# Kernel optimization log

Measured on AMD Instinct MI355X. Metric: run time of the kernel, lower is better.

The kernel has to match this reference:

```python
import jax, jax.numpy as jnp
import numpy as np

EPS = 1e-05

def _q(a):
    # 'bfloat16' set_precision: round to bf16, compute in fp32
    return a.astype(jnp.bfloat16).astype(jnp.float32)

def setup_inputs() -> dict:
    key = jax.random.key(0)
    k1, k2 = jax.random.split(key)
    B, C, H, W = 64, 128, 56, 56
    x = jax.random.normal(k1, (B, C, H, W), dtype=jnp.float32)
    gamma = jax.random.uniform(k2, (C,), dtype=jnp.float32)
    beta = jnp.zeros((C,), dtype=jnp.float32)
    return {"x": x, "gamma": gamma, "beta": beta, "num_chunks": 8}

def reference(x, gamma, beta, num_chunks):
    B, C, H, W = x.shape
    x = _q(x)
    g = _q(gamma)
    # (C, num_chunks, B*H*W/num_chunks): channel-major flatten then chunk
    y = jnp.transpose(x, (1, 0, 2, 3)).reshape(C, num_chunks, -1)
    chunk_size = y.shape[-1]
    sum_max = _q(y.max(-1).sum(-1))            # [C]
    sum_min = _q(y.min(-1).sum(-1))            # [C]
    avg_max = _q(sum_max / num_chunks)
    avg_min = _q(sum_min / num_chunks)
    total = _q(y.reshape(C, -1).sum(-1))       # [C]
    n = B * H * W
    avg = _q(total / n)
    scale_fix = 1.0 / (2.0 * np.log(chunk_size)) ** 0.5
    scale = _q(1.0 / ((avg_max - avg_min) * scale_fix + EPS))
    avg = avg.reshape(1, C, 1, 1)
    scale = scale.reshape(1, C, 1, 1)
    out = _q((x - avg) * scale)
    out = _q(out * g.reshape(1, C, 1, 1) + beta.reshape(1, C, 1, 1))
    return out
```

## Files before the change

kernel.cpp:

```cpp
#include <hip/hip_runtime.h>
#include <hip/hip_bf16.h>
#include <math.h>

constexpr int HW = 56 * 56;

__device__ __forceinline__ float qbf(float f) {
    unsigned u = __float_as_uint(f);
    u += 0x7fffu + ((u >> 16) & 1u);
    u &= 0xffff0000u;
    return __uint_as_float(u);
}

__global__ __launch_bounds__(256) void stats_kernel(
    const float* __restrict__ x, const int* __restrict__ nch_p,
    int C, int n,
    float* __restrict__ ws_max, float* __restrict__ ws_min, float* __restrict__ ws_sum)
{
    const int nch = *nch_p;
    const int cs  = n / nch;
    const int P   = C * nch;

    __shared__ float smax[4], smin[4], ssum[4];

    for (int p = blockIdx.x; p < P; p += gridDim.x) {
        const int c = p / nch;
        const int j = p - c * nch;

        float vmax = -INFINITY, vmin = INFINITY, vsum = 0.f;

        if ((cs & 3) == 0) {
            const int cs4 = cs >> 2;
            for (int t = threadIdx.x; t < cs4; t += blockDim.x) {
                const int f = j * cs + 4 * t;
                const int b = f / HW;
                const int r = f - b * HW;
                const float4 v = *reinterpret_cast<const float4*>(
                    x + ((size_t)b * C + c) * HW + r);
                const float a0 = qbf(v.x), a1 = qbf(v.y), a2 = qbf(v.z), a3 = qbf(v.w);
                vmax = fmaxf(vmax, fmaxf(fmaxf(a0, a1), fmaxf(a2, a3)));
                vmin = fminf(vmin, fminf(fminf(a0, a1), fminf(a2, a3)));
                vsum += (a0 + a1) + (a2 + a3);
            }
        } else {
            for (int t = threadIdx.x; t < cs; t += blockDim.x) {
                const int f = j * cs + t;
                const int b = f / HW;
                const int r = f - b * HW;
                const float a = qbf(x[((size_t)b * C + c) * HW + r]);
                vmax = fmaxf(vmax, a);
                vmin = fminf(vmin, a);
                vsum += a;
            }
        }

        #pragma unroll
        for (int off = 32; off > 0; off >>= 1) {
            vmax = fmaxf(vmax, __shfl_xor(vmax, off));
            vmin = fminf(vmin, __shfl_xor(vmin, off));
            vsum += __shfl_xor(vsum, off);
        }
        const int wave = threadIdx.x >> 6;
        if ((threadIdx.x & 63) == 0) { smax[wave] = vmax; smin[wave] = vmin; ssum[wave] = vsum; }
        __syncthreads();
        if (threadIdx.x == 0) {
            float m = smax[0], mi = smin[0], s = ssum[0];
            const int nw = blockDim.x >> 6;
            for (int w = 1; w < nw; ++w) {
                m = fmaxf(m, smax[w]); mi = fminf(mi, smin[w]); s += ssum[w];
            }
            ws_max[p] = m; ws_min[p] = mi; ws_sum[p] = s;
        }
        __syncthreads();
    }
}

__global__ __launch_bounds__(256) void finalize_kernel(
    const float* __restrict__ ws_max, const float* __restrict__ ws_min,
    const float* __restrict__ ws_sum, const int* __restrict__ nch_p,
    int C, int n, float* __restrict__ avg_out, float* __restrict__ scale_out)
{
    const int c = blockIdx.x * blockDim.x + threadIdx.x;
    if (c >= C) return;
    const int nch = *nch_p;

    float smax = 0.f, smin = 0.f, stot = 0.f;
    for (int j = 0; j < nch; ++j) {
        smax += ws_max[c * nch + j];
        smin += ws_min[c * nch + j];
        stot += ws_sum[c * nch + j];
    }
    smax = qbf(smax);
    smin = qbf(smin);
    const float avg_max = qbf(smax / (float)nch);
    const float avg_min = qbf(smin / (float)nch);
    const float total   = qbf(stot);
    const float avg     = qbf(total / (float)n);

    const int cs = n / nch;
    const double sf_d = 1.0 / sqrt(2.0 * log((double)cs));
    const float scale_fix = (float)sf_d;
    const float scale = qbf(1.0f / ((avg_max - avg_min) * scale_fix + 1e-5f));

    avg_out[c]   = avg;
    scale_out[c] = scale;
}

__global__ __launch_bounds__(256) void norm_kernel(
    const float* __restrict__ x, const float* __restrict__ gamma,
    const float* __restrict__ beta, const float* __restrict__ avg,
    const float* __restrict__ scale, int C, long total, float* __restrict__ out)
{
    const long total4 = total >> 2;
    const long stride = (long)gridDim.x * blockDim.x;
    for (long i4 = (long)blockIdx.x * blockDim.x + threadIdx.x; i4 < total4; i4 += stride) {
        const long i = i4 << 2;
        const int  c = (int)((i / HW) % C);
        const float a = avg[c], s = scale[c], g = qbf(gamma[c]), bt = beta[c];
        const float4 v = *reinterpret_cast<const float4*>(x + i);
        float4 o;
        o.x = qbf(qbf((qbf(v.x) - a) * s) * g + bt);
        o.y = qbf(qbf((qbf(v.y) - a) * s) * g + bt);
        o.z = qbf(qbf((qbf(v.z) - a) * s) * g + bt);
        o.w = qbf(qbf((qbf(v.w) - a) * s) * g + bt);
        *reinterpret_cast<float4*>(out + i) = o;
    }
    const long rem_start = total4 << 2;
    if (blockIdx.x == 0) {
        for (long i = rem_start + threadIdx.x; i < total; i += blockDim.x) {
            const int c = (int)((i / HW) % C);
            const float a = avg[c], s = scale[c], g = qbf(gamma[c]), bt = beta[c];
            out[i] = qbf(qbf((qbf(x[i]) - a) * s) * g + bt);
        }
    }
}

extern "C" void kernel_launch(void* const* d_in, const int* in_sizes, int n_in,
                              void* d_out, int out_size, void* d_ws, size_t ws_size,
                              hipStream_t stream) {
    const float* x     = (const float*)d_in[0];
    const float* gamma = (const float*)d_in[1];
    const float* beta  = (const float*)d_in[2];
    const int*   nch_p = (const int*)d_in[3];
    float* out = (float*)d_out;

    const int  C     = in_sizes[1];
    const long total = (long)in_sizes[0];
    const int  n     = (int)(total / C);

    constexpr int Pmax = 4096, Cmax = 1024;
    float* ws_f   = (float*)d_ws;
    float* ws_max = ws_f;
    float* ws_min = ws_f + Pmax;
    float* ws_sum = ws_f + 2 * Pmax;
    float* avg    = ws_f + 3 * Pmax;
    float* scale  = ws_f + 3 * Pmax + Cmax;

    stats_kernel<<<1024, 256, 0, stream>>>(x, nch_p, C, n, ws_max, ws_min, ws_sum);
    finalize_kernel<<<(C + 255) / 256, 256, 0, stream>>>(ws_max, ws_min, ws_sum,
                                                         nch_p, C, n, avg, scale);
    norm_kernel<<<2048, 256, 0, stream>>>(x, gamma, beta, avg, scale, C, total, out);
}
```

Baseline: 201.7 us.

## Fuse stats, finalize and normalize into one cooperative kernel with grid syncs

Replaces the three separate launches with a single cooperative kernel that computes per-chunk stats, grid-syncs, has block 0 finalize per-channel avg/scale, grid-syncs again, then normalizes. It also switches to plane-wise indexing in both stats and normalize passes, which avoids per-element divisions by HW, and the normalize pass hoists per-channel parameters out of the inner loop. This removes launch gaps and may let x stay partly in cache between passes. In exchange it adds two grid-wide barriers, a serial finalize step on one block, and a fixed 1024-block grid that must be co-resident.

```diff
diff --git a/kernel.cpp b/kernel.cpp
--- a/kernel.cpp
+++ b/kernel.cpp
@@ -1,8 +1,12 @@
 #include <hip/hip_runtime.h>
 #include <hip/hip_bf16.h>
+#include <hip/hip_cooperative_groups.h>
 #include <math.h>
 
-constexpr int HW = 56 * 56;
+namespace cg = cooperative_groups;
+
+constexpr int HW  = 56 * 56;
+constexpr int HW4 = HW / 4;
 
 __device__ __forceinline__ float qbf(float f) {
     unsigned u = __float_as_uint(f);
@@ -11,16 +15,30 @@
     return __uint_as_float(u);
 }
 
-__global__ __launch_bounds__(256) void stats_kernel(
-    const float* __restrict__ x, const int* __restrict__ nch_p,
-    int C, int n,
-    float* __restrict__ ws_max, float* __restrict__ ws_min, float* __restrict__ ws_sum)
+constexpr int WS_MAX = 0;
+constexpr int WS_MIN = 4096;
+constexpr int WS_SUM = 8192;
+constexpr int WS_AVG = 12288;
+constexpr int WS_SCL = 13312;
+
+__global__ __launch_bounds__(256, 4) void fused_kernel(
+    const float* __restrict__ x, const float* __restrict__ gamma,
+    const float* __restrict__ beta, const int* __restrict__ nch_p,
+    int C, int n, unsigned total, float* __restrict__ ws, float* __restrict__ out)
 {
     const int nch = *nch_p;
     const int cs  = n / nch;
     const int P   = C * nch;
 
+    float* ws_max = ws + WS_MAX;
+    float* ws_min = ws + WS_MIN;
+    float* ws_sum = ws + WS_SUM;
+    float* avgv   = ws + WS_AVG;
+    float* sclv   = ws + WS_SCL;
+
     __shared__ float smax[4], smin[4], ssum[4];
+
+    const bool plane_mode = (cs % HW == 0) && ((total % (unsigned)HW) == 0u);
 
     for (int p = blockIdx.x; p < P; p += gridDim.x) {
         const int c = p / nch;
@@ -28,14 +46,15 @@
 
         float vmax = -INFINITY, vmin = INFINITY, vsum = 0.f;
 
-        if ((cs & 3) == 0) {
-            const int cs4 = cs >> 2;
-            for (int t = threadIdx.x; t < cs4; t += blockDim.x) {
-                const int f = j * cs + 4 * t;
-                const int b = f / HW;
-                const int r = f - b * HW;
+        if (plane_mode) {
+            const int ppc  = cs / HW;
+            const int b0   = j * ppc;
+            const int tot4 = ppc * HW4;
+            for (int t = threadIdx.x; t < tot4; t += blockDim.x) {
+                const int b = t / HW4;
+                const int r = t - b * HW4;
                 const float4 v = *reinterpret_cast<const float4*>(
-                    x + ((size_t)b * C + c) * HW + r);
+                    x + ((size_t)(b0 + b) * C + c) * HW + 4 * r);
                 const float a0 = qbf(v.x), a1 = qbf(v.y), a2 = qbf(v.z), a3 = qbf(v.w);
                 vmax = fmaxf(vmax, fmaxf(fmaxf(a0, a1), fmaxf(a2, a3)));
                 vmin = fminf(vmin, fminf(fminf(a0, a1), fminf(a2, a3)));
@@ -64,71 +83,62 @@
         __syncthreads();
         if (threadIdx.x == 0) {
             float m = smax[0], mi = smin[0], s = ssum[0];
-            const int nw = blockDim.x >> 6;
-            for (int w = 1; w < nw; ++w) {
+            for (int w = 1; w < 4; ++w) {
                 m = fmaxf(m, smax[w]); mi = fminf(mi, smin[w]); s += ssum[w];
             }
             ws_max[p] = m; ws_min[p] = mi; ws_sum[p] = s;
         }
         __syncthreads();
     }
-}
 
-__global__ __launch_bounds__(256) void finalize_kernel(
-    const float* __restrict__ ws_max, const float* __restrict__ ws_min,
-    const float* __restrict__ ws_sum, const int* __restrict__ nch_p,
-    int C, int n, float* __restrict__ avg_out, float* __restrict__ scale_out)
-{
-    const int c = blockIdx.x * blockDim.x + threadIdx.x;
-    if (c >= C) return;
-    const int nch = *nch_p;
+    cg::this_grid().sync();
 
-    float smax = 0.f, smin = 0.f, stot = 0.f;
-    for (int j = 0; j < nch; ++j) {
-        smax += ws_max[c * nch + j];
-        smin += ws_min[c * nch + j];
-        stot += ws_sum[c * nch + j];
+    if (blockIdx.x == 0) {
+        for (int c = threadIdx.x; c < C; c += blockDim.x) {
+            float smx = 0.f, smn = 0.f, stot = 0.f;
+            for (int j = 0; j < nch; ++j) {
+                smx  += ws_max[c * nch + j];
+                smn  += ws_min[c * nch + j];
+                stot += ws_sum[c * nch + j];
+            }
+            smx = qbf(smx);
+            smn = qbf(smn);
+            const float avg_max = qbf(smx / (float)nch);
+            const float avg_min = qbf(smn / (float)nch);
+            const float tq      = qbf(stot);
+            const float avg     = qbf(tq / (float)n);
+            const double sf_d   = 1.0 / sqrt(2.0 * log((double)cs));
+            const float scale_fix = (float)sf_d;
+            const float scale = qbf(1.0f / ((avg_max - avg_min) * scale_fix + 1e-5f));
+            avgv[c] = avg;
+            sclv[c] = scale;
+        }
     }
-    smax = qbf(smax);
-    smin = qbf(smin);
-    const float avg_max = qbf(smax / (float)nch);
-    const float avg_min = qbf(smin / (float)nch);
-    const float total   = qbf(stot);
-    const float avg     = qbf(total / (float)n);
 
-    const int cs = n / nch;
-    const double sf_d = 1.0 / sqrt(2.0 * log((double)cs));
-    const float scale_fix = (float)sf_d;
-    const float scale = qbf(1.0f / ((avg_max - avg_min) * scale_fix + 1e-5f));
+    cg::this_grid().sync();
 
-    avg_out[c]   = avg;
-    scale_out[c] = scale;
-}
-
-__global__ __launch_bounds__(256) void norm_kernel(
-    const float* __restrict__ x, const float* __restrict__ gamma,
-    const float* __restrict__ beta, const float* __restrict__ avg,
-    const float* __restrict__ scale, int C, long total, float* __restrict__ out)
-{
-    const long total4 = total >> 2;
-    const long stride = (long)gridDim.x * blockDim.x;
-    for (long i4 = (long)blockIdx.x * blockDim.x + threadIdx.x; i4 < total4; i4 += stride) {
-        const long i = i4 << 2;
-        const int  c = (int)((i / HW) % C);
-        const float a = avg[c], s = scale[c], g = qbf(gamma[c]), bt = beta[c];
-        const float4 v = *reinterpret_cast<const float4*>(x + i);
-        float4 o;
-        o.x = qbf(qbf((qbf(v.x) - a) * s) * g + bt);
-        o.y = qbf(qbf((qbf(v.y) - a) * s) * g + bt);
-        o.z = qbf(qbf((qbf(v.z) - a) * s) * g + bt);
-        o.w = qbf(qbf((qbf(v.w) - a) * s) * g + bt);
-        *reinterpret_cast<float4*>(out + i) = o;
-    }
-    const long rem_start = total4 << 2;
-    if (blockIdx.x == 0) {
-        for (long i = rem_start + threadIdx.x; i < total; i += blockDim.x) {
-            const int c = (int)((i / HW) % C);
-            const float a = avg[c], s = scale[c], g = qbf(gamma[c]), bt = beta[c];
+    if (plane_mode) {
+        const int planes = (int)(total / (unsigned)HW);
+        for (int pl = blockIdx.x; pl < planes; pl += gridDim.x) {
+            const int c = pl % C;
+            const float a = avgv[c], s = sclv[c], g = qbf(gamma[c]), bt = beta[c];
+            const float* xp = x   + (size_t)pl * HW;
+            float*       op = out + (size_t)pl * HW;
+            for (int t = threadIdx.x; t < HW4; t += blockDim.x) {
+                const float4 v = *reinterpret_cast<const float4*>(xp + 4 * t);
+                float4 o;
+                o.x = qbf(qbf((qbf(v.x) - a) * s) * g + bt);
+                o.y = qbf(qbf((qbf(v.y) - a) * s) * g + bt);
+                o.z = qbf(qbf((qbf(v.z) - a) * s) * g + bt);
+                o.w = qbf(qbf((qbf(v.w) - a) * s) * g + bt);
+                *reinterpret_cast<float4*>(op + 4 * t) = o;
+            }
+        }
+    } else {
+        const unsigned stride = gridDim.x * blockDim.x;
+        for (unsigned i = blockIdx.x * blockDim.x + threadIdx.x; i < total; i += stride) {
+            const int c = (int)((i / (unsigned)HW) % (unsigned)C);
+            const float a = avgv[c], s = sclv[c], g = qbf(gamma[c]), bt = beta[c];
             out[i] = qbf(qbf((qbf(x[i]) - a) * s) * g + bt);
         }
     }
@@ -141,22 +151,15 @@
     const float* gamma = (const float*)d_in[1];
     const float* beta  = (const float*)d_in[2];
     const int*   nch_p = (const int*)d_in[3];
-    float* out = (float*)d_out;
+    float* outp = (float*)d_out;
+    float* ws   = (float*)d_ws;
 
-    const int  C     = in_sizes[1];
-    const long total = (long)in_sizes[0];
-    const int  n     = (int)(total / C);
+    const int      C     = in_sizes[1];
+    const unsigned total = (unsigned)in_sizes[0];
+    const int      n     = (int)(total / (unsigned)C);
 
-    constexpr int Pmax = 4096, Cmax = 1024;
-    float* ws_f   = (float*)d_ws;
-    float* ws_max = ws_f;
-    float* ws_min = ws_f + Pmax;
-    float* ws_sum = ws_f + 2 * Pmax;
-    float* avg    = ws_f + 3 * Pmax;
-    float* scale  = ws_f + 3 * Pmax + Cmax;
-
-    stats_kernel<<<1024, 256, 0, stream>>>(x, nch_p, C, n, ws_max, ws_min, ws_sum);
-    finalize_kernel<<<(C + 255) / 256, 256, 0, stream>>>(ws_max, ws_min, ws_sum,
-                                                         nch_p, C, n, avg, scale);
-    norm_kernel<<<2048, 256, 0, stream>>>(x, gamma, beta, avg, scale, C, total, out);
+    void* args[] = { (void*)&x, (void*)&gamma, (void*)&beta, (void*)&nch_p,
+                     (void*)&C, (void*)&n, (void*)&total, (void*)&ws, (void*)&outp };
+    hipLaunchCooperativeKernel((void*)fused_kernel, dim3(1024), dim3(256),
+                               args, 0, stream);
 }
```

New measurement: 408.5 us. 103% more time.
